# Optimization experiments

Hardware: AMD Instinct MI355X
Metric: run time of the kernel (lower is better)

## Reference

```python
import jax, jax.numpy as jnp
import numpy as np

APERTURE = 128
LN_EPS = 1e-6

def _layer_norm(y, g, b):
    mu = jnp.mean(y, axis=-1, keepdims=True)
    var = jnp.var(y, axis=-1, keepdims=True)
    return (y - mu) / jnp.sqrt(var + LN_EPS) * g + b

def setup_inputs() -> dict:
    key = jax.random.key(0)
    ks = jax.random.split(key, 12)
    B, S, D = 4, 4096, 1024
    gain = np.sqrt(2.0)
    xav = lambda k, fan_out, fan_in: jax.random.uniform(
        k, (fan_out, fan_in), jnp.float32,
        -gain * np.sqrt(6.0 / (fan_in + fan_out)), gain * np.sqrt(6.0 / (fan_in + fan_out)))
    return {
        "x": jax.random.normal(ks[0], (B, S, D), jnp.float32),
        "Wq": xav(ks[1], D, D),
        "Wk": xav(ks[2], D, D),
        "Wv": xav(ks[3], D, D),
        "Wo": xav(ks[4], D, D),
        "k1_w": xav(ks[5], D, D),
        "k1_b": jnp.full((D,), 0.1, jnp.float32),
        "k2_w": xav(ks[6], 1, D),
        "k2_b": jnp.full((1,), 0.1, jnp.float32),
        "ln_g": jnp.ones((D,), jnp.float32),
        "ln_b": jnp.zeros((D,), jnp.float32),
    }

def reference(x, Wq, Wk, Wv, Wo, k1_w, k1_b, k2_w, k2_b, ln_g, ln_b):
    B, S, D = x.shape
    scale = jnp.float32(1.0 / np.sqrt(D))
    neg_inf = jnp.float32(-np.inf)

    Q = x @ Wq.T  # [B,S,D]
    K = x @ Wk.T
    V = x @ Wv.T

    e = jnp.einsum('bsd,btd->bst', Q, K) * scale  # [B,S,S]

    # ignore_self: -inf on the diagonal
    i = jnp.arange(S)[:, None]
    j = jnp.arange(S)[None, :]
    e = jnp.where(i == j, neg_inf, e)

    # banded aperture mask: tril(e, ap) * triu(e, -ap); zeros of the product -> -inf
    d = j - i
    scope = jnp.where(d <= APERTURE, e, 0.0) * jnp.where(d >= -APERTURE, e, 0.0)
    e = jnp.where(scope == 0.0, neg_inf, e)

    alpha = jax.nn.softmax(e, axis=2)
    c = jnp.einsum('bst,btd->bsd', alpha, V)
    c = c @ Wo.T

    y = c + x
    y = _layer_norm(y, ln_g, ln_b)
    y = jax.nn.relu(y @ k1_w.T + k1_b)
    y = _layer_norm(y, ln_g, ln_b)
    y = jax.nn.sigmoid(y @ k2_w.T + k2_b)  # [B,S,1]
    return y.reshape(B, S)
```

## Files before the change

kernel.cpp:

```cpp
#include <hip/hip_runtime.h>
#include <math.h>

#define DD 1024
#define SS 4096
#define AP 128
#define LN_EPS 1e-6f
#define BK 32
#define BAND 384

typedef __bf16 bf16;
typedef __attribute__((ext_vector_type(4))) __bf16 bf16x4;
typedef __attribute__((ext_vector_type(8))) __bf16 bf16x8;
typedef __attribute__((ext_vector_type(4))) float f32x4;

#define GLOAD_LDS16(g, l)                                                   \
    __builtin_amdgcn_global_load_lds(                                        \
        (const __attribute__((address_space(1))) void*)(g),                  \
        (__attribute__((address_space(3))) void*)(l), 16, 0, 0)

__global__ __launch_bounds__(256) void prep_all(const float* __restrict__ x,
                                                const float* __restrict__ Wq,
                                                const float* __restrict__ Wk,
                                                const float* __restrict__ Wv,
                                                const float* __restrict__ Wo,
                                                const float* __restrict__ k1w,
                                                const float* __restrict__ k1b,
                                                const float* __restrict__ lng,
                                                const float* __restrict__ lnb,
                                                bf16* __restrict__ xb,
                                                bf16* __restrict__ Wob,
                                                bf16* __restrict__ k1g,
                                                bf16* __restrict__ Wtb,
                                                float* __restrict__ u1,
                                                float* __restrict__ c1b) {
    __shared__ float tile[64][65];
    const int bid = blockIdx.x;
    const int tid = threadIdx.x;
    if (bid < 16384) {
        const int i = (bid * 256 + tid) * 4;
        const float4 a = *(const float4*)(x + i);
        bf16x4 o;
        o[0] = (__bf16)a.x; o[1] = (__bf16)a.y; o[2] = (__bf16)a.z; o[3] = (__bf16)a.w;
        *(bf16x4*)(xb + i) = o;
        return;
    }
    if (bid < 18432) {
        const int b2 = bid - 16384;
        const int sel = b2 >> 10;
        const int bb = b2 & 1023;
        const float* s = sel ? k1w : Wo;
        bf16* d = sel ? k1g : Wob;
        const int i = (bb * 256 + tid) * 4;
        float4 a = *(const float4*)(s + i);
        if (sel) {
            const float4 g4 = *(const float4*)(lng + (i & (DD - 1)));
            a.x *= g4.x; a.y *= g4.y; a.z *= g4.z; a.w *= g4.w;
        }
        bf16x4 o;
        o[0] = (__bf16)a.x; o[1] = (__bf16)a.y; o[2] = (__bf16)a.z; o[3] = (__bf16)a.w;
        *(bf16x4*)(d + i) = o;
        return;
    }
    if (bid < 19200) {
        const int t = bid - 18432;
        const int tz = t >> 8;
        const int tb_ = t & 255;
        const float* in = (tz == 0) ? Wq : (tz == 1) ? Wk : Wv;
        bf16* out = Wtb + ((size_t)tz << 20);
        const int r0 = (tb_ >> 4) * 64, c0 = (tb_ & 15) * 64;
        const int lr = tid >> 4;
        const int lc = (tid & 15) * 4;
#pragma unroll
        for (int rr = 0; rr < 4; rr++) {
            const int row = lr + rr * 16;
            const float4 v = *(const float4*)(in + (size_t)(r0 + row) * DD + c0 + lc);
            tile[row][lc] = v.x; tile[row][lc + 1] = v.y;
            tile[row][lc + 2] = v.z; tile[row][lc + 3] = v.w;
        }
        __syncthreads();
#pragma unroll
        for (int rr = 0; rr < 4; rr++) {
            const int row = lr + rr * 16;
            bf16x4 o;
            o[0] = (__bf16)tile[lc + 0][row];
            o[1] = (__bf16)tile[lc + 1][row];
            o[2] = (__bf16)tile[lc + 2][row];
            o[3] = (__bf16)tile[lc + 3][row];
            *(bf16x4*)(out + (size_t)(c0 + row) * DD + r0 + lc) = o;
        }
        return;
    }
    const int pv = bid - 19200;
    const int lane = tid & 63, wave = tid >> 6;
    const int n = pv * 4 + wave;
    const float* row = k1w + (size_t)n * DD + lane * 16;
    float su = 0.f, sb = 0.f;
#pragma unroll
    for (int q = 0; q < 4; q++) {
        const float4 a = *(const float4*)(row + q * 4);
        const float4 g4 = *(const float4*)(lng + lane * 16 + q * 4);
        const float4 b4 = *(const float4*)(lnb + lane * 16 + q * 4);
        su += a.x * g4.x + a.y * g4.y + a.z * g4.z + a.w * g4.w;
        sb += a.x * b4.x + a.y * b4.y + a.z * b4.z + a.w * b4.w;
    }
#pragma unroll
    for (int off = 32; off > 0; off >>= 1) {
        su += __shfl_xor(su, off);
        sb += __shfl_xor(sb, off);
    }
    if (lane == 0) {
        u1[n] = su;
        c1b[n] = sb + k1b[n];
    }
}

__global__ __launch_bounds__(256) void gemm_pair(const bf16* __restrict__ A0,
                                                 const bf16* __restrict__ W0,
                                                 bf16* __restrict__ O0,
                                                 const bf16* __restrict__ A1,
                                                 const bf16* __restrict__ W1,
                                                 bf16* __restrict__ O1) {
    const bf16* A = blockIdx.z ? A1 : A0;
    const bf16* W = blockIdx.z ? W1 : W0;
    bf16* O = blockIdx.z ? O1 : O0;
    __shared__ bf16 As[128 * BK];
    __shared__ bf16 Bs[128 * BK];
    const int tid = threadIdx.x;
    const int lane = tid & 63;
    const int wave = tid >> 6;
    const int wm = wave & 1;
    const int wn = wave >> 1;
    const int m0 = blockIdx.y * 128;
    const int n0 = blockIdx.x * 128;

    const int c = wave * 64 + lane;
    const int ar = c >> 2;
    const int ac = (c & 3) << 3;
    char* AsB = (char*)As;
    char* BsB = (char*)Bs;
    const int lr = lane & 15;
    const int lk = (lane >> 4) << 3;

    f32x4 acc[4][4] = {};

    for (int kt = 0; kt < DD; kt += BK) {
        const bf16* ga0 = A + (size_t)(m0 + ar) * DD + kt + ac;
        const bf16* gb0 = W + (size_t)(n0 + ar) * DD + kt + ac;
        GLOAD_LDS16(ga0, AsB + wave * 1024);
        GLOAD_LDS16(ga0 + (size_t)64 * DD, AsB + 4096 + wave * 1024);
        GLOAD_LDS16(gb0, BsB + wave * 1024);
        GLOAD_LDS16(gb0 + (size_t)64 * DD, BsB + 4096 + wave * 1024);
        __syncthreads();

        bf16x8 af[4], bfr[4];
#pragma unroll
        for (int i = 0; i < 4; i++)
            af[i] = *(const bf16x8*)&As[(wm * 64 + i * 16 + lr) * BK + lk];
#pragma unroll
        for (int j = 0; j < 4; j++)
            bfr[j] = *(const bf16x8*)&Bs[(wn * 64 + j * 16 + lr) * BK + lk];
#pragma unroll
        for (int i = 0; i < 4; i++)
#pragma unroll
            for (int j = 0; j < 4; j++)
                acc[i][j] = __builtin_amdgcn_mfma_f32_16x16x32_bf16(af[i], bfr[j], acc[i][j], 0, 0, 0);
        __syncthreads();
    }

#pragma unroll
    for (int i = 0; i < 4; i++) {
        const int row = m0 + wm * 64 + i * 16 + ((lane >> 4) << 2);
#pragma unroll
        for (int j = 0; j < 4; j++) {
            const int col = n0 + wn * 64 + j * 16 + (lane & 15);
#pragma unroll
            for (int rr = 0; rr < 4; rr++)
                O[(size_t)(row + rr) * DD + col] = (__bf16)acc[i][j][rr];
        }
    }
}

__global__ __launch_bounds__(512) void gemm_uv(const bf16* __restrict__ xb,
                                               const bf16* __restrict__ Gt,
                                               const bf16* __restrict__ W2,
                                               bf16* __restrict__ Ub,
                                               bf16* __restrict__ Vt2) {
    __shared__ bf16 As[256 * BK];
    __shared__ bf16 Bs[128 * BK];
    int id = blockIdx.x;
    const bf16* A;
    const bf16* W;
    bf16* O;
    int m0, n0, ldo;
    if (id < 512) {
        A = xb; W = Gt; O = Ub;
        m0 = (id & 63) * 256; n0 = (id >> 6) * 128; ldo = DD;
    } else {
        id -= 512;
        A = W2; W = xb; O = Vt2;
        m0 = (id >> 7) * 256; n0 = (id & 127) * 128; ldo = 4 * SS;
    }
    const int tid = threadIdx.x;
    const int lane = tid & 63;
    const int wave = tid >> 6;
    const int wm = wave & 3;
    const int wn = wave >> 2;

    const int ar = tid >> 2;
    const int ac = (tid & 3) << 3;
    char* AsB = (char*)As;
    char* BsB = (char*)Bs;
    const int lr = lane & 15;
    const int lk = (lane >> 4) << 3;

    f32x4 acc[4][4] = {};

    for (int kt = 0; kt < DD; kt += BK) {
        const bf16* ga0 = A + (size_t)(m0 + ar) * DD + kt + ac;
        const bf16* gb0 = W + (size_t)(n0 + ar) * DD + kt + ac;
        GLOAD_LDS16(ga0, AsB + wave * 1024);
        GLOAD_LDS16(ga0 + (size_t)128 * DD, AsB + 8192 + wave * 1024);
        GLOAD_LDS16(gb0, BsB + wave * 1024);
        __syncthreads();

        bf16x8 af[4], bfr[4];
#pragma unroll
        for (int i = 0; i < 4; i++)
            af[i] = *(const bf16x8*)&As[(wm * 64 + i * 16 + lr) * BK + lk];
#pragma unroll
        for (int j = 0; j < 4; j++)
            bfr[j] = *(const bf16x8*)&Bs[(wn * 64 + j * 16 + lr) * BK + lk];
#pragma unroll
        for (int i = 0; i < 4; i++)
#pragma unroll
            for (int j = 0; j < 4; j++)
                acc[i][j] = __builtin_amdgcn_mfma_f32_16x16x32_bf16(af[i], bfr[j], acc[i][j], 0, 0, 0);
        __syncthreads();
    }

#pragma unroll
    for (int i = 0; i < 4; i++) {
        const int row = m0 + wm * 64 + i * 16 + ((lane >> 4) << 2);
#pragma unroll
        for (int j = 0; j < 4; j++) {
            const int col = n0 + wn * 64 + j * 16 + (lane & 15);
#pragma unroll
            for (int rr = 0; rr < 4; rr++)
                O[(size_t)(row + rr) * ldo + col] = (__bf16)acc[i][j][rr];
        }
    }
}

__global__ __launch_bounds__(512) void gemm_k1(const bf16* __restrict__ T,
                                               const bf16* __restrict__ k1g,
                                               const float* __restrict__ part_t,
                                               const float* __restrict__ u1,
                                               const float* __restrict__ c1b,
                                               const float* __restrict__ lng,
                                               const float* __restrict__ k2w,
                                               float* __restrict__ part_h) {
    __shared__ bf16 As[256 * BK];
    __shared__ bf16 Bs[128 * BK];
    __shared__ float lmu[256], lrs[256];
    const int m0 = blockIdx.x * 256;
    const int n0 = blockIdx.y * 128;
    const int tid = threadIdx.x;
    const int lane = tid & 63;
    const int wave = tid >> 6;
    const int wm = wave & 3;
    const int wn = wave >> 2;

    const int ar = tid >> 2;
    const int ac = (tid & 3) << 3;
    char* AsB = (char*)As;
    char* BsB = (char*)Bs;
    const int lr = lane & 15;
    const int lk = (lane >> 4) << 3;

    if (tid < 256) {
        const float* p = part_t + (size_t)(m0 + tid) * 32;
        float s1 = 0.f, s2 = 0.f;
#pragma unroll
        for (int s = 0; s < 8; s++) {
            const float4 v = *(const float4*)(p + s * 4);
            s1 += v.x + v.z;
            s2 += v.y + v.w;
        }
        const float m = s1 * (1.f / DD);
        lmu[tid] = m;
        lrs[tid] = rsqrtf(s2 * (1.f / DD) - m * m + LN_EPS);
    }

    f32x4 acc[4][4] = {};

    for (int kt = 0; kt < DD; kt += BK) {
        const bf16* ga0 = T + (size_t)(m0 + ar) * DD + kt + ac;
        const bf16* gb0 = k1g + (size_t)(n0 + ar) * DD + kt + ac;
        GLOAD_LDS16(ga0, AsB + wave * 1024);
        GLOAD_LDS16(ga0 + (size_t)128 * DD, AsB + 8192 + wave * 1024);
        GLOAD_LDS16(gb0, BsB + wave * 1024);
        __syncthreads();

        bf16x8 af[4], bfr[4];
#pragma unroll
        for (int i = 0; i < 4; i++)
            af[i] = *(const bf16x8*)&As[(wm * 64 + i * 16 + lr) * BK + lk];
#pragma unroll
        for (int j = 0; j < 4; j++)
            bfr[j] = *(const bf16x8*)&Bs[(wn * 64 + j * 16 + lr) * BK + lk];
#pragma unroll
        for (int i = 0; i < 4; i++)
#pragma unroll
            for (int j = 0; j < 4; j++)
                acc[i][j] = __builtin_amdgcn_mfma_f32_16x16x32_bf16(af[i], bfr[j], acc[i][j], 0, 0, 0);
        __syncthreads();
    }

    float u1v[4], cbv[4], ugv[4];
#pragma unroll
    for (int j = 0; j < 4; j++) {
        const int col = n0 + wn * 64 + j * 16 + (lane & 15);
        u1v[j] = u1[col];
        cbv[j] = c1b[col];
        ugv[j] = lng[col] * k2w[col];
    }
    const int strip = blockIdx.y * 2 + wn;
#pragma unroll
    for (int i = 0; i < 4; i++) {
#pragma unroll
        for (int rr = 0; rr < 4; rr++) {
            const int lrow = wm * 64 + i * 16 + ((lane >> 4) << 2) + rr;
            const int row = m0 + lrow;
            const float mr = lmu[lrow], rs = lrs[lrow];
            float s1 = 0.f, s2 = 0.f, s3 = 0.f;
#pragma unroll
            for (int j = 0; j < 4; j++) {
                const float v = rs * (acc[i][j][rr] - mr * u1v[j]) + cbv[j];
                const float h = fmaxf(v, 0.f);
                s1 += h; s2 += h * h; s3 += h * ugv[j];
            }
#pragma unroll
            for (int off = 8; off > 0; off >>= 1) {
                s1 += __shfl_xor(s1, off);
                s2 += __shfl_xor(s2, off);
                s3 += __shfl_xor(s3, off);
            }
            if ((lane & 15) == 0) {
                float* p = part_h + (size_t)row * 48 + strip * 3;
                p[0] = s1; p[1] = s2; p[2] = s3;
            }
        }
    }
}

__global__ __launch_bounds__(256) void attn_s_mfma(const bf16* __restrict__ U,
                                                   const bf16* __restrict__ X,
                                                   float* __restrict__ S) {
    __shared__ bf16 As[128 * BK];
    __shared__ bf16 Bs[128 * BK];
    const int tid = threadIdx.x;
    const int lane = tid & 63;
    const int wave = tid >> 6;
    const int wm = wave & 1;
    const int wn = wave >> 1;
    const int t = blockIdx.x;
    const int nb = blockIdx.y;
    const int m0 = t * 128;
    const long w0 = (long)t * 128 - 128 + (long)nb * 128;

    const int c = wave * 64 + lane;
    const int ar = c >> 2;
    const int ac = (c & 3) << 3;
    char* AsB = (char*)As;
    char* BsB = (char*)Bs;
    const int lr = lane & 15;
    const int lk = (lane >> 4) << 3;

    f32x4 acc[4][4] = {};

    for (int kt = 0; kt < DD; kt += BK) {
        const bf16* ga0 = U + (size_t)(m0 + ar) * DD + kt + ac;
        const bf16* gb0 = X + (w0 + ar) * DD + kt + ac;
        GLOAD_LDS16(ga0, AsB + wave * 1024);
        GLOAD_LDS16(ga0 + (size_t)64 * DD, AsB + 4096 + wave * 1024);
        GLOAD_LDS16(gb0, BsB + wave * 1024);
        GLOAD_LDS16(gb0 + (size_t)64 * DD, BsB + 4096 + wave * 1024);
        __syncthreads();

        bf16x8 af[4], bfr[4];
#pragma unroll
        for (int i = 0; i < 4; i++)
            af[i] = *(const bf16x8*)&As[(wm * 64 + i * 16 + lr) * BK + lk];
#pragma unroll
        for (int j = 0; j < 4; j++)
            bfr[j] = *(const bf16x8*)&Bs[(wn * 64 + j * 16 + lr) * BK + lk];
#pragma unroll
        for (int i = 0; i < 4; i++)
#pragma unroll
            for (int j = 0; j < 4; j++)
                acc[i][j] = __builtin_amdgcn_mfma_f32_16x16x32_bf16(af[i], bfr[j], acc[i][j], 0, 0, 0);
        __syncthreads();
    }

#pragma unroll
    for (int i = 0; i < 4; i++) {
        const int row = m0 + wm * 64 + i * 16 + ((lane >> 4) << 2);
#pragma unroll
        for (int j = 0; j < 4; j++) {
            const int col = nb * 128 + wn * 64 + j * 16 + (lane & 15);
#pragma unroll
            for (int rr = 0; rr < 4; rr++)
                S[(size_t)(row + rr) * BAND + col] = acc[i][j][rr];
        }
    }
}

__global__ __launch_bounds__(256) void attn_softmax(const float* __restrict__ S,
                                                    bf16* __restrict__ P) {
    const int wave = threadIdx.x >> 6;
    const int lane = threadIdx.x & 63;
    const int g = blockIdx.x * 4 + wave;
    const int i = g & (SS - 1);
    const int j_start = ((i >> 7) << 7) - 128;
    const float scale = 0.03125f;
    float s[6];
    float m = -INFINITY;
#pragma unroll
    for (int t = 0; t < 6; t++) {
        const int jj = lane + t * 64;
        const int j = j_start + jj;
        const int dj = j - i;
        const bool valid = (j >= 0) && (j < SS) && (dj != 0) && (dj <= AP) && (dj >= -AP);
        const float v = S[(size_t)g * BAND + jj] * scale;
        s[t] = valid ? v : -INFINITY;
        m = fmaxf(m, s[t]);
    }
#pragma unroll
    for (int off = 32; off > 0; off >>= 1) m = fmaxf(m, __shfl_xor(m, off));
    float l = 0.f;
#pragma unroll
    for (int t = 0; t < 6; t++) {
        s[t] = __expf(s[t] - m);
        l += s[t];
    }
#pragma unroll
    for (int off = 32; off > 0; off >>= 1) l += __shfl_xor(l, off);
    const float inv = 1.f / l;
#pragma unroll
    for (int t = 0; t < 6; t++)
        P[(size_t)g * BAND + lane + t * 64] = (__bf16)(s[t] * inv);
}

__global__ __launch_bounds__(512) void attn_pv_mfma(const bf16* __restrict__ P,
                                                    const bf16* __restrict__ Vt,
                                                    const bf16* __restrict__ xres,
                                                    bf16* __restrict__ T,
                                                    float* __restrict__ part_t) {
    __shared__ bf16 As[128 * BK];
    __shared__ bf16 Bs[256 * BK];
    const int tid = threadIdx.x;
    const int lane = tid & 63;
    const int wave = tid >> 6;
    const int wm = wave & 1;
    const int wn = wave >> 1;
    const int t = blockIdx.x;
    const int m0 = t * 128;
    const int n0 = blockIdx.y * 256;
    const bf16* Wb = Vt + (long)t * 128 - 128;

    const int ar = tid >> 2;
    const int ac = (tid & 3) << 3;
    char* AsB = (char*)As;
    char* BsB = (char*)Bs;
    const int lr = lane & 15;
    const int lk = (lane >> 4) << 3;

    f32x4 acc[4][4] = {};

    for (int kt = 0; kt < BAND; kt += BK) {
        const bf16* ga0 = P + (size_t)(m0 + ar) * BAND + kt + ac;
        const bf16* gb0 = Wb + (size_t)(n0 + ar) * (4 * SS) + kt + ac;
        GLOAD_LDS16(ga0, AsB + wave * 1024);
        GLOAD_LDS16(gb0, BsB + wave * 1024);
        GLOAD_LDS16(gb0 + (size_t)128 * (4 * SS), BsB + 8192 + wave * 1024);
        __syncthreads();

        bf16x8 af[4], bfr[4];
#pragma unroll
        for (int i = 0; i < 4; i++)
            af[i] = *(const bf16x8*)&As[(wm * 64 + i * 16 + lr) * BK + lk];
#pragma unroll
        for (int j = 0; j < 4; j++)
            bfr[j] = *(const bf16x8*)&Bs[(wn * 64 + j * 16 + lr) * BK + lk];
#pragma unroll
        for (int i = 0; i < 4; i++)
#pragma unroll
            for (int j = 0; j < 4; j++)
                acc[i][j] = __builtin_amdgcn_mfma_f32_16x16x32_bf16(af[i], bfr[j], acc[i][j], 0, 0, 0);
        __syncthreads();
    }

    const int strip = blockIdx.y * 4 + wn;
#pragma unroll
    for (int i = 0; i < 4; i++) {
#pragma unroll
        for (int rr = 0; rr < 4; rr++) {
            const int row = m0 + wm * 64 + i * 16 + ((lane >> 4) << 2) + rr;
            float s1 = 0.f, s2 = 0.f;
#pragma unroll
            for (int j = 0; j < 4; j++) {
                const int col = n0 + wn * 64 + j * 16 + (lane & 15);
                const size_t idx = (size_t)row * DD + col;
                const __bf16 tv_b = (__bf16)(acc[i][j][rr] + (float)xres[idx]);
                T[idx] = tv_b;
                const float tv = (float)tv_b;
                s1 += tv; s2 += tv * tv;
            }
#pragma unroll
            for (int off = 8; off > 0; off >>= 1) {
                s1 += __shfl_xor(s1, off);
                s2 += __shfl_xor(s2, off);
            }
            if ((lane & 15) == 0) {
                float2 st; st.x = s1; st.y = s2;
                *(float2*)(part_t + (size_t)row * 32 + strip * 2) = st;
            }
        }
    }
}

__global__ __launch_bounds__(256) void ln_k2_p(const float* __restrict__ part_h,
                                               const float* __restrict__ g,
                                               const float* __restrict__ bta,
                                               const float* __restrict__ w2,
                                               const float* __restrict__ b2,
                                               float* __restrict__ out) {
    __shared__ float red[256], red2[256];
    const int tid = threadIdx.x;
    const float4 g4 = *(const float4*)(g + tid * 4);
    const float4 w4 = *(const float4*)(w2 + tid * 4);
    const float4 b4 = *(const float4*)(bta + tid * 4);
    red[tid] = g4.x * w4.x + g4.y * w4.y + g4.z * w4.z + g4.w * w4.w;
    red2[tid] = b4.x * w4.x + b4.y * w4.y + b4.z * w4.z + b4.w * w4.w;
    __syncthreads();
    for (int s = 128; s > 0; s >>= 1) {
        if (tid < s) { red[tid] += red[tid + s]; red2[tid] += red2[tid + s]; }
        __syncthreads();
    }
    const float sum_u = red[0];
    const float sum_bw = red2[0];

    const int r = blockIdx.x * 256 + tid;
    const float* p = part_h + (size_t)r * 48;
    float s1 = 0.f, s2 = 0.f, s3 = 0.f;
#pragma unroll
    for (int s = 0; s < 16; s++) {
        s1 += p[s * 3 + 0];
        s2 += p[s * 3 + 1];
        s3 += p[s * 3 + 2];
    }
    const float m = s1 * (1.f / DD);
    const float var = s2 * (1.f / DD) - m * m;
    const float rs = rsqrtf(var + LN_EPS);
    const float z = rs * (s3 - m * sum_u) + sum_bw + b2[0];
    out[r] = 1.f / (1.f + __expf(-z));
}

extern "C" void kernel_launch(void* const* d_in, const int* in_sizes, int n_in,
                              void* d_out, int out_size, void* d_ws, size_t ws_size,
                              hipStream_t stream) {
    const float* x   = (const float*)d_in[0];
    const float* Wq  = (const float*)d_in[1];
    const float* Wk  = (const float*)d_in[2];
    const float* Wv  = (const float*)d_in[3];
    const float* Wo  = (const float*)d_in[4];
    const float* k1w = (const float*)d_in[5];
    const float* k1b = (const float*)d_in[6];
    const float* k2w = (const float*)d_in[7];
    const float* k2b = (const float*)d_in[8];
    const float* lng = (const float*)d_in[9];
    const float* lnb = (const float*)d_in[10];
    float* out = (float*)d_out;

    const int N = 4 * SS;
    char* ws = (char*)d_ws;
    bf16*  Ub   = (bf16*)(ws);
    bf16*  xb   = (bf16*)(ws + ((size_t)32  << 20));
    bf16*  Vt2  = (bf16*)(ws + ((size_t)64  << 20));
    bf16*  P    = (bf16*)(ws + ((size_t)96  << 20));
    float* S    = (float*)(ws + ((size_t)108 << 20));
    bf16*  T    = (bf16*)(ws + ((size_t)164 << 20));
    bf16*  Wtb  = (bf16*)(ws + ((size_t)196 << 20));
    bf16*  Wqtb = Wtb;
    bf16*  Wktb = Wqtb + (1 << 20);
    bf16*  Wvtb = Wktb + (1 << 20);
    bf16*  Wob  = Wvtb + (1 << 20);
    bf16*  k1g  = Wob  + (1 << 20);
    bf16*  Gtb  = k1g  + (1 << 20);
    bf16*  W2b  = Gtb  + (1 << 20);
    float* u1     = (float*)(ws + ((size_t)210 << 20));
    float* c1b    = u1 + DD;
    float* part_t = (float*)(ws + ((size_t)211 << 20));
    float* part_h = (float*)(ws + ((size_t)214 << 20));

    dim3 tb(256);

    prep_all<<<19456, tb, 0, stream>>>(x, Wq, Wk, Wv, Wo, k1w, k1b, lng, lnb,
                                       xb, Wob, k1g, Wtb, u1, c1b);

    gemm_pair<<<dim3(8, 8, 2), tb, 0, stream>>>(Wktb, Wqtb, Gtb, Wob, Wvtb, W2b);

    gemm_uv<<<1024, dim3(512), 0, stream>>>(xb, Gtb, W2b, Ub, Vt2);

    attn_s_mfma<<<dim3(N / 128, 3), tb, 0, stream>>>(Ub, xb, S);
    attn_softmax<<<N / 4, tb, 0, stream>>>(S, P);
    attn_pv_mfma<<<dim3(N / 128, 4), dim3(512), 0, stream>>>(P, Vt2, xb, T, part_t);

    gemm_k1<<<dim3(64, 8), dim3(512), 0, stream>>>(T, k1g, part_t, u1, c1b, lng, k2w, part_h);
    ln_k2_p<<<N / 256, tb, 0, stream>>>(part_h, lng, lnb, k2w, k2b, out);
}
```

Before: 339.9 us.

## Use 256x256 tiles with double-buffered LDS pipeline in uv and k1 GEMMs

Replaces the 256x128, BK=32 single-buffer GEMM loops in gemm_uv and gemm_k1 with a shared kloop256 routine. It computes 256x256 tiles using K-steps of 64 in two halves, double-buffered in 128KB of LDS with an XOR swizzle. Global loads for the next stages are interleaved with the MFMA work, guarded by partial vmcnt waits and setprio hints, so load latency and barriers overlap compute and each operand is reused more. The cost is fewer blocks (512 and 256), higher register and LDS use, and one block per CU.

```diff
diff --git a/kernel.cpp b/kernel.cpp
--- a/kernel.cpp
+++ b/kernel.cpp
@@ -180,73 +180,132 @@
     }
 }
 
+
+#define KL_STAGE_A(tt, hh, bb)                                               \
+    {                                                                        \
+        const bf16* gp_ = Aop + gofsA + (tt) * 64 + (hh) * 32;               \
+        GLOAD_LDS16(gp_, smem + (bb) + (hh) * 16384 + ldsW);                 \
+        GLOAD_LDS16(gp_ + (size_t)128 * DD,                                  \
+                    smem + (bb) + (hh) * 16384 + 8192 + ldsW);               \
+    }
+#define KL_STAGE_B(tt, hh, bb)                                               \
+    {                                                                        \
+        const bf16* gp_ = Bop + gofsB + (tt) * 64 + (hh) * 32;               \
+        GLOAD_LDS16(gp_, smem + (bb) + 32768 + (hh) * 16384 + ldsW);         \
+        GLOAD_LDS16(gp_ + (size_t)128 * DD,                                  \
+                    smem + (bb) + 32768 + (hh) * 16384 + 8192 + ldsW);       \
+    }
+#define KL_READS_A(ks, mh)                                                   \
+    af[0] = *(const bf16x8*)(sA + bufo + (ks) * 16384 + (mh) * 4096);        \
+    af[1] = *(const bf16x8*)(sA + bufo + (ks) * 16384 + (mh) * 4096 + 1024); \
+    af[2] = *(const bf16x8*)(sA + bufo + (ks) * 16384 + (mh) * 4096 + 2048); \
+    af[3] = *(const bf16x8*)(sA + bufo + (ks) * 16384 + (mh) * 4096 + 3072);
+#define KL_READS_B(ks)                                                       \
+    bfr[0] = *(const bf16x8*)(sB + bufo + (ks) * 16384);                     \
+    bfr[1] = *(const bf16x8*)(sB + bufo + (ks) * 16384 + 1024);              \
+    bfr[2] = *(const bf16x8*)(sB + bufo + (ks) * 16384 + 2048);              \
+    bfr[3] = *(const bf16x8*)(sB + bufo + (ks) * 16384 + 3072);
+#define KL_MFMA4(I, MH)                                                      \
+    acc[(MH) * 4 + I][0] = __builtin_amdgcn_mfma_f32_16x16x32_bf16(af[I], bfr[0], acc[(MH) * 4 + I][0], 0, 0, 0); \
+    acc[(MH) * 4 + I][1] = __builtin_amdgcn_mfma_f32_16x16x32_bf16(af[I], bfr[1], acc[(MH) * 4 + I][1], 0, 0, 0); \
+    acc[(MH) * 4 + I][2] = __builtin_amdgcn_mfma_f32_16x16x32_bf16(af[I], bfr[2], acc[(MH) * 4 + I][2], 0, 0, 0); \
+    acc[(MH) * 4 + I][3] = __builtin_amdgcn_mfma_f32_16x16x32_bf16(af[I], bfr[3], acc[(MH) * 4 + I][3], 0, 0, 0);
+#define KL_MFMA16(MH)                                                        \
+    __builtin_amdgcn_s_setprio(1);                                           \
+    KL_MFMA4(0, MH) KL_MFMA4(1, MH) KL_MFMA4(2, MH) KL_MFMA4(3, MH)          \
+    __builtin_amdgcn_s_setprio(0);
+#define KL_BARRIER(N) asm volatile("s_waitcnt vmcnt(" #N ")\n\ts_barrier" ::: "memory")
+
+__device__ __forceinline__ void kloop256(const bf16* __restrict__ Aop,
+                                         const bf16* __restrict__ Bop,
+                                         const int m0, const int n0,
+                                         char* smem, f32x4 (&acc)[8][4],
+                                         const int tid, const int lane,
+                                         const int wave, const int wm, const int wn) {
+    const int grow = tid >> 2;
+    const int gslot = (tid & 3) ^ ((tid >> 3) & 3);
+    const size_t gofsA = (size_t)(m0 + grow) * DD + gslot * 8;
+    const size_t gofsB = (size_t)(n0 + grow) * DD + gslot * 8;
+    const int ldsW = wave * 1024;
+    const int sxo = (((lane >> 4) ^ ((lane >> 1) & 3)) << 4);
+    const char* sA = smem + wm * 8192 + (lane & 15) * 64 + sxo;
+    const char* sB = smem + 32768 + wn * 4096 + (lane & 15) * 64 + sxo;
+
+    bf16x8 af[4], bfr[4];
+
+    KL_STAGE_A(0, 0, 0) KL_STAGE_B(0, 0, 0)
+    KL_STAGE_A(0, 1, 0) KL_STAGE_B(0, 1, 0)
+    KL_STAGE_A(1, 0, 65536) KL_STAGE_B(1, 0, 65536)
+
+    int bufo = 0;
+    for (int t = 0; t < 15; t++) {
+        const int nb = bufo ^ 65536;
+        KL_BARRIER(8);
+        KL_READS_A(0, 0) KL_READS_B(0)
+        KL_STAGE_A(t + 1, 1, nb)
+        KL_MFMA16(0)
+        KL_READS_A(0, 1)
+        KL_STAGE_B(t + 1, 1, nb)
+        KL_MFMA16(1)
+        KL_BARRIER(8);
+        KL_READS_A(1, 0) KL_READS_B(1)
+        if (t < 14) { KL_STAGE_A(t + 2, 0, bufo) }
+        KL_MFMA16(0)
+        KL_READS_A(1, 1)
+        if (t < 14) { KL_STAGE_B(t + 2, 0, bufo) }
+        KL_MFMA16(1)
+        bufo = nb;
+    }
+    KL_BARRIER(4);
+    KL_READS_A(0, 0) KL_READS_B(0)
+    KL_MFMA16(0)
+    KL_READS_A(0, 1)
+    KL_MFMA16(1)
+    KL_BARRIER(0);
+    KL_READS_A(1, 0) KL_READS_B(1)
+    KL_MFMA16(0)
+    KL_READS_A(1, 1)
+    KL_MFMA16(1)
+}
+
 __global__ __launch_bounds__(512) void gemm_uv(const bf16* __restrict__ xb,
                                                const bf16* __restrict__ Gt,
                                                const bf16* __restrict__ W2,
                                                bf16* __restrict__ Ub,
                                                bf16* __restrict__ Vt2) {
-    __shared__ bf16 As[256 * BK];
-    __shared__ bf16 Bs[128 * BK];
+    __shared__ char smem[131072];
     int id = blockIdx.x;
     const bf16* A;
     const bf16* W;
     bf16* O;
-    int m0, n0, ldo;
-    if (id < 512) {
+    int m0, n0;
+    size_t ldo;
+    if (id < 256) {
         A = xb; W = Gt; O = Ub;
-        m0 = (id & 63) * 256; n0 = (id >> 6) * 128; ldo = DD;
+        m0 = (id & 63) * 256; n0 = (id >> 6) * 256; ldo = DD;
     } else {
-        id -= 512;
+        id -= 256;
         A = W2; W = xb; O = Vt2;
-        m0 = (id >> 7) * 256; n0 = (id & 127) * 128; ldo = 4 * SS;
+        m0 = (id >> 6) * 256; n0 = (id & 63) * 256; ldo = (size_t)4 * SS;
     }
     const int tid = threadIdx.x;
     const int lane = tid & 63;
     const int wave = tid >> 6;
-    const int wm = wave & 3;
-    const int wn = wave >> 2;
-
-    const int ar = tid >> 2;
-    const int ac = (tid & 3) << 3;
-    char* AsB = (char*)As;
-    char* BsB = (char*)Bs;
-    const int lr = lane & 15;
-    const int lk = (lane >> 4) << 3;
-
-    f32x4 acc[4][4] = {};
-
-    for (int kt = 0; kt < DD; kt += BK) {
-        const bf16* ga0 = A + (size_t)(m0 + ar) * DD + kt + ac;
-        const bf16* gb0 = W + (size_t)(n0 + ar) * DD + kt + ac;
-        GLOAD_LDS16(ga0, AsB + wave * 1024);
-        GLOAD_LDS16(ga0 + (size_t)128 * DD, AsB + 8192 + wave * 1024);
-        GLOAD_LDS16(gb0, BsB + wave * 1024);
-        __syncthreads();
-
-        bf16x8 af[4], bfr[4];
-#pragma unroll
-        for (int i = 0; i < 4; i++)
-            af[i] = *(const bf16x8*)&As[(wm * 64 + i * 16 + lr) * BK + lk];
-#pragma unroll
-        for (int j = 0; j < 4; j++)
-            bfr[j] = *(const bf16x8*)&Bs[(wn * 64 + j * 16 + lr) * BK + lk];
-#pragma unroll
-        for (int i = 0; i < 4; i++)
-#pragma unroll
-            for (int j = 0; j < 4; j++)
-                acc[i][j] = __builtin_amdgcn_mfma_f32_16x16x32_bf16(af[i], bfr[j], acc[i][j], 0, 0, 0);
-        __syncthreads();
-    }
-
-#pragma unroll
-    for (int i = 0; i < 4; i++) {
-        const int row = m0 + wm * 64 + i * 16 + ((lane >> 4) << 2);
+    const int wm = wave & 1;
+    const int wn = wave >> 1;
+
+    f32x4 acc[8][4] = {};
+    kloop256(A, W, m0, n0, smem, acc, tid, lane, wave, wm, wn);
+
+#pragma unroll
+    for (int a = 0; a < 8; a++) {
+        const int row = m0 + wm * 128 + a * 16 + ((lane >> 4) << 2);
 #pragma unroll
         for (int j = 0; j < 4; j++) {
             const int col = n0 + wn * 64 + j * 16 + (lane & 15);
 #pragma unroll
             for (int rr = 0; rr < 4; rr++)
-                O[(size_t)(row + rr) * ldo + col] = (__bf16)acc[i][j][rr];
+                O[(size_t)(row + rr) * ldo + col] = (__bf16)acc[a][j][rr];
         }
     }
 }
@@ -259,23 +318,15 @@
                                                const float* __restrict__ lng,
                                                const float* __restrict__ k2w,
                                                float* __restrict__ part_h) {
-    __shared__ bf16 As[256 * BK];
-    __shared__ bf16 Bs[128 * BK];
+    __shared__ char smem[131072];
     __shared__ float lmu[256], lrs[256];
     const int m0 = blockIdx.x * 256;
-    const int n0 = blockIdx.y * 128;
+    const int n0 = blockIdx.y * 256;
     const int tid = threadIdx.x;
     const int lane = tid & 63;
     const int wave = tid >> 6;
-    const int wm = wave & 3;
-    const int wn = wave >> 2;
-
-    const int ar = tid >> 2;
-    const int ac = (tid & 3) << 3;
-    char* AsB = (char*)As;
-    char* BsB = (char*)Bs;
-    const int lr = lane & 15;
-    const int lk = (lane >> 4) << 3;
+    const int wm = wave & 1;
+    const int wn = wave >> 1;
 
     if (tid < 256) {
         const float* p = part_t + (size_t)(m0 + tid) * 32;
@@ -290,31 +341,10 @@
         lmu[tid] = m;
         lrs[tid] = rsqrtf(s2 * (1.f / DD) - m * m + LN_EPS);
     }
-
-    f32x4 acc[4][4] = {};
-
-    for (int kt = 0; kt < DD; kt += BK) {
-        const bf16* ga0 = T + (size_t)(m0 + ar) * DD + kt + ac;
-        const bf16* gb0 = k1g + (size_t)(n0 + ar) * DD + kt + ac;
-        GLOAD_LDS16(ga0, AsB + wave * 1024);
-        GLOAD_LDS16(ga0 + (size_t)128 * DD, AsB + 8192 + wave * 1024);
-        GLOAD_LDS16(gb0, BsB + wave * 1024);
-        __syncthreads();
-
-        bf16x8 af[4], bfr[4];
-#pragma unroll
-        for (int i = 0; i < 4; i++)
-            af[i] = *(const bf16x8*)&As[(wm * 64 + i * 16 + lr) * BK + lk];
-#pragma unroll
-        for (int j = 0; j < 4; j++)
-            bfr[j] = *(const bf16x8*)&Bs[(wn * 64 + j * 16 + lr) * BK + lk];
-#pragma unroll
-        for (int i = 0; i < 4; i++)
-#pragma unroll
-            for (int j = 0; j < 4; j++)
-                acc[i][j] = __builtin_amdgcn_mfma_f32_16x16x32_bf16(af[i], bfr[j], acc[i][j], 0, 0, 0);
-        __syncthreads();
-    }
+    __syncthreads();
+
+    f32x4 acc[8][4] = {};
+    kloop256(T, k1g, m0, n0, smem, acc, tid, lane, wave, wm, wn);
 
     float u1v[4], cbv[4], ugv[4];
 #pragma unroll
@@ -324,18 +354,18 @@
         cbv[j] = c1b[col];
         ugv[j] = lng[col] * k2w[col];
     }
-    const int strip = blockIdx.y * 2 + wn;
-#pragma unroll
-    for (int i = 0; i < 4; i++) {
+    const int strip = blockIdx.y * 4 + wn;
+#pragma unroll
+    for (int a = 0; a < 8; a++) {
 #pragma unroll
         for (int rr = 0; rr < 4; rr++) {
-            const int lrow = wm * 64 + i * 16 + ((lane >> 4) << 2) + rr;
+            const int lrow = wm * 128 + a * 16 + ((lane >> 4) << 2) + rr;
             const int row = m0 + lrow;
             const float mr = lmu[lrow], rs = lrs[lrow];
             float s1 = 0.f, s2 = 0.f, s3 = 0.f;
 #pragma unroll
             for (int j = 0; j < 4; j++) {
-                const float v = rs * (acc[i][j][rr] - mr * u1v[j]) + cbv[j];
+                const float v = rs * (acc[a][j][rr] - mr * u1v[j]) + cbv[j];
                 const float h = fmaxf(v, 0.f);
                 s1 += h; s2 += h * h; s3 += h * ugv[j];
             }
@@ -610,12 +640,12 @@
 
     gemm_pair<<<dim3(8, 8, 2), tb, 0, stream>>>(Wktb, Wqtb, Gtb, Wob, Wvtb, W2b);
 
-    gemm_uv<<<1024, dim3(512), 0, stream>>>(xb, Gtb, W2b, Ub, Vt2);
+    gemm_uv<<<512, dim3(512), 0, stream>>>(xb, Gtb, W2b, Ub, Vt2);
 
     attn_s_mfma<<<dim3(N / 128, 3), tb, 0, stream>>>(Ub, xb, S);
     attn_softmax<<<N / 4, tb, 0, stream>>>(S, P);
     attn_pv_mfma<<<dim3(N / 128, 4), dim3(512), 0, stream>>>(P, Vt2, xb, T, part_t);
 
-    gemm_k1<<<dim3(64, 8), dim3(512), 0, stream>>>(T, k1g, part_t, u1, c1b, lng, k2w, part_h);
+    gemm_k1<<<dim3(64, 4), dim3(512), 0, stream>>>(T, k1g, part_t, u1, c1b, lng, k2w, part_h);
     ln_k2_p<<<N / 256, tb, 0, stream>>>(part_h, lng, lnb, k2w, k2b, out);
 }
```

After: 334.2 us. Within noise of the previous version (-1.7%).
